# Kernel tuning notes

Hardware: AMD Instinct MI355X
Metric: run time of the kernel (lower is better)

Reference implementation:

```python
import jax, jax.numpy as jnp
import numpy as np

B = 8388608  # batch


def setup_inputs() -> dict:
    key = jax.random.key(0)
    ks = jax.random.split(key, 5)
    x = jax.random.uniform(ks[0], (B, 2), dtype=jnp.float32)
    # QuasiPolyLayer fc1: 2x2 grid of synapses, each with power (init 1.0) and term_weights[3]
    fc1_tw = jax.random.normal(ks[1], (2, 2, 3), dtype=jnp.float32)   # [out, in, terms]
    fc1_power = jnp.ones((2, 2), dtype=jnp.float32)                   # init power = 1
    fc1_bias = jax.random.normal(ks[2], (2,), dtype=jnp.float32)
    # Network4Infra: 4 synapses (add1, add2, prod1, prod2), bias3 scalar
    m4_tw = jax.random.normal(ks[3], (4, 3), dtype=jnp.float32)
    m4_power = jnp.ones((4,), dtype=jnp.float32)
    m4_bias3 = jax.random.normal(ks[4], (1,), dtype=jnp.float32)
    return {"x": x, "fc1_tw": fc1_tw, "fc1_power": fc1_power, "fc1_bias": fc1_bias,
            "m4_tw": m4_tw, "m4_power": m4_power, "m4_bias3": m4_bias3}


def _synapse(x, tw0, p):
    # QuasiPolySynapse with power=1 init: extra-term loop range(1, min(floor(p)-1, 3)) is empty
    return tw0 * x ** p


def reference(x, fc1_tw, fc1_power, fc1_bias, m4_tw, m4_power, m4_bias3):
    # fc1: y[:, i] = sum_j tw0[i, j] * x[:, j] ** power[i, j]  + bias[i]
    pw = x[:, None, :] ** fc1_power[None, :, :]                # [B, out=2, in=2]
    h = jnp.sum(fc1_tw[None, :, :, 0] * pw, axis=2) + fc1_bias  # [B, 2]
    h = jax.nn.sigmoid(h)
    # Network4Infra
    x0, x1 = h[:, 0], h[:, 1]
    s1 = _synapse(x0, m4_tw[0, 0], m4_power[0])
    s2 = _synapse(x1, m4_tw[1, 0], m4_power[1])
    p1 = _synapse(x0, m4_tw[2, 0], m4_power[2])
    p2 = _synapse(x1, m4_tw[3, 0], m4_power[3])
    prod = (s1 + s2 + p1 * p2 + m4_bias3[0])[:, None]          # [B, 1]
    return jax.nn.sigmoid(prod)
```

## Files before the change

### kernel.cpp

```cpp
#include <hip/hip_runtime.h>


typedef float vfloat4 __attribute__((ext_vector_type(4)));
typedef float vfloat2 __attribute__((ext_vector_type(2)));

__device__ __forceinline__ float sigmoid_fast(float z) {
    float t = __expf(-z);
    return __builtin_amdgcn_rcpf(1.0f + t);
}
__device__ __forceinline__ float sigmoid_exact(float z) {
    return 1.0f / (1.0f + expf(-z));
}
__device__ __forceinline__ float pw(float x, float p) {
    return (p == 1.0f) ? x : __powf(x, p);
}

__global__ __launch_bounds__(256) void net24_kernel(
    const float* __restrict__ x,
    float* __restrict__ out,
    const float* __restrict__ fc1_tw,
    const float* __restrict__ fc1_power,
    const float* __restrict__ fc1_bias,
    const float* __restrict__ m4_tw,
    const float* __restrict__ m4_power,
    const float* __restrict__ m4_bias3,
    int n)
{
    const float tw00 = fc1_tw[0], tw01 = fc1_tw[3], tw10 = fc1_tw[6], tw11 = fc1_tw[9];
    const float p00 = fc1_power[0], p01 = fc1_power[1], p10 = fc1_power[2], p11 = fc1_power[3];
    const float b0 = fc1_bias[0], b1 = fc1_bias[1];
    const float m0 = m4_tw[0], m1 = m4_tw[3], m2 = m4_tw[6], m3 = m4_tw[9];
    const float q0 = m4_power[0], q1 = m4_power[1], q2 = m4_power[2], q3 = m4_power[3];
    const float bias3 = m4_bias3[0];

    const bool all_pow1 = (p00 == 1.0f) & (p01 == 1.0f) & (p10 == 1.0f) & (p11 == 1.0f) &
                          (q0 == 1.0f) & (q1 == 1.0f) & (q2 == 1.0f) & (q3 == 1.0f);

    auto eval_fast = [&](float x0, float x1) -> float {
        float h0 = sigmoid_fast(fmaf(tw00, x0, fmaf(tw01, x1, b0)));
        float h1 = sigmoid_fast(fmaf(tw10, x0, fmaf(tw11, x1, b1)));
        float s  = fmaf(m0, h0, fmaf(m1, h1, bias3));
        s = fmaf(m2 * h0, m3 * h1, s);
        return sigmoid_fast(s);
    };
    auto eval_gen = [&](float x0, float x1) -> float {
        float h0 = sigmoid_exact(fmaf(tw00, pw(x0, p00), fmaf(tw01, pw(x1, p01), b0)));
        float h1 = sigmoid_exact(fmaf(tw10, pw(x0, p10), fmaf(tw11, pw(x1, p11), b1)));
        float s  = fmaf(m0, pw(h0, q0), fmaf(m1, pw(h1, q1), bias3));
        s = fmaf(m2 * pw(h0, q2), m3 * pw(h1, q3), s);
        return sigmoid_exact(s);
    };

    const int gid  = blockIdx.x * blockDim.x + threadIdx.x;
    const int wave = gid >> 6;
    const int lane = gid & 63;
    const long long rowbase = (long long)wave * 256;
    if (rowbase >= n) return;

    if (all_pow1 && rowbase + 256 <= n) {
        const vfloat4* xv = (const vfloat4*)(x + rowbase * 2);
        vfloat4 a = xv[lane];
        vfloat4 b = xv[64 + lane];
        vfloat2 ra, rb;
        ra.x = eval_fast(a.x, a.y);
        ra.y = eval_fast(a.z, a.w);
        rb.x = eval_fast(b.x, b.y);
        rb.y = eval_fast(b.z, b.w);
        *(vfloat2*)(out + rowbase + 2 * lane)       = ra;
        *(vfloat2*)(out + rowbase + 128 + 2 * lane) = rb;
    } else {
        for (long long r = rowbase + lane; r < rowbase + 256 && r < n; r += 64) {
            out[r] = eval_gen(x[r * 2], x[r * 2 + 1]);
        }
    }
}

extern "C" void kernel_launch(void* const* d_in, const int* in_sizes, int n_in,
                              void* d_out, int out_size, void* d_ws, size_t ws_size,
                              hipStream_t stream) {
    const float* x         = (const float*)d_in[0];
    const float* fc1_tw    = (const float*)d_in[1];
    const float* fc1_power = (const float*)d_in[2];
    const float* fc1_bias  = (const float*)d_in[3];
    const float* m4_tw     = (const float*)d_in[4];
    const float* m4_power  = (const float*)d_in[5];
    const float* m4_bias3  = (const float*)d_in[6];
    float* out = (float*)d_out;

    const int n = out_size;
    const long long waves = ((long long)n + 255) / 256;
    const long long threads = waves * 64;
    const int block = 256;
    const long long grid = (threads + block - 1) / block;

    net24_kernel<<<(int)grid, block, 0, stream>>>(x, out, fc1_tw, fc1_power, fc1_bias,
                                                  m4_tw, m4_power, m4_bias3, n);
}
```

Measured before the change: 107.6 us.

## Use persistent grid-stride waves with register prefetch and nontemporal stores

Replaces the one-tile-per-wave launch with a fixed grid of up to 2048 blocks. Each wave walks tiles in a grid-stride loop and loads the next tile's inputs before computing the current one, so memory latency overlaps with compute. Outputs are written with nontemporal stores to avoid polluting the cache. The trade-off is fewer waves in flight, relying on in-register prefetch rather than occupancy to hide latency on a purely bandwidth-bound stream.

```diff
diff --git a/kernel.cpp b/kernel.cpp
--- a/kernel.cpp
+++ b/kernel.cpp
@@ -51,26 +51,48 @@
         return sigmoid_exact(s);
     };
 
-    const int gid  = blockIdx.x * blockDim.x + threadIdx.x;
-    const int wave = gid >> 6;
-    const int lane = gid & 63;
-    const long long rowbase = (long long)wave * 256;
-    if (rowbase >= n) return;
+    const int gid   = blockIdx.x * blockDim.x + threadIdx.x;
+    const int wave  = gid >> 6;
+    const int lane  = gid & 63;
+    const int nwaves = (gridDim.x * blockDim.x) >> 6;
+    const long long ntiles = ((long long)n + 255) >> 8;
 
-    if (all_pow1 && rowbase + 256 <= n) {
-        const vfloat4* xv = (const vfloat4*)(x + rowbase * 2);
-        vfloat4 a = xv[lane];
-        vfloat4 b = xv[64 + lane];
-        vfloat2 ra, rb;
-        ra.x = eval_fast(a.x, a.y);
-        ra.y = eval_fast(a.z, a.w);
-        rb.x = eval_fast(b.x, b.y);
-        rb.y = eval_fast(b.z, b.w);
-        *(vfloat2*)(out + rowbase + 2 * lane)       = ra;
-        *(vfloat2*)(out + rowbase + 128 + 2 * lane) = rb;
+    if (all_pow1 && (n & 255) == 0) {
+        long long t = wave;
+        if (t >= ntiles) return;
+
+        const vfloat4* xv0 = (const vfloat4*)(x + (t << 9));
+        vfloat4 a0 = xv0[lane];
+        vfloat4 b0 = xv0[64 + lane];
+
+        while (true) {
+            const long long tn = t + nwaves;
+            vfloat4 a1, b1;
+            const bool more = tn < ntiles;
+            if (more) {
+                const vfloat4* xv1 = (const vfloat4*)(x + (tn << 9));
+                a1 = xv1[lane];
+                b1 = xv1[64 + lane];
+            }
+
+            vfloat2 ra, rb;
+            ra.x = eval_fast(a0.x, a0.y);
+            ra.y = eval_fast(a0.z, a0.w);
+            rb.x = eval_fast(b0.x, b0.y);
+            rb.y = eval_fast(b0.z, b0.w);
+            float* o = out + (t << 8);
+            __builtin_nontemporal_store(ra, (vfloat2*)(o + 2 * lane));
+            __builtin_nontemporal_store(rb, (vfloat2*)(o + 128 + 2 * lane));
+
+            if (!more) break;
+            t = tn; a0 = a1; b0 = b1;
+        }
     } else {
-        for (long long r = rowbase + lane; r < rowbase + 256 && r < n; r += 64) {
-            out[r] = eval_gen(x[r * 2], x[r * 2 + 1]);
+        for (long long t = wave; t < ntiles; t += nwaves) {
+            const long long rowbase = t << 8;
+            for (long long r = rowbase + lane; r < rowbase + 256 && r < n; r += 64) {
+                out[r] = eval_gen(x[r * 2], x[r * 2 + 1]);
+            }
         }
     }
 }
@@ -88,11 +110,13 @@
     float* out = (float*)d_out;
 
     const int n = out_size;
-    const long long waves = ((long long)n + 255) / 256;
-    const long long threads = waves * 64;
-    const int block = 256;
-    const long long grid = (threads + block - 1) / block;
+    const long long ntiles = ((long long)n + 255) / 256;
+    long long blocks = 2048;
+    const long long waves_needed = ntiles;
+    const long long max_blocks = (waves_needed + 3) / 4;
+    if (blocks > max_blocks) blocks = max_blocks;
+    if (blocks < 1) blocks = 1;
 
-    net24_kernel<<<(int)grid, block, 0, stream>>>(x, out, fc1_tw, fc1_power, fc1_bias,
+    net24_kernel<<<(int)blocks, 256, 0, stream>>>(x, out, fc1_tw, fc1_power, fc1_bias,
                                                   m4_tw, m4_power, m4_bias3, n);
 }
```

Result: slower. 115.5 us (+7.3%).
